# Optimization experiments

Measured on AMD Instinct MI355X. Metric: run time of the kernel, lower is better.

Reference implementation:

```python
import jax, jax.numpy as jnp
import numpy as np

EMBED_DIM = 256
NUM_HEADS = 8
HEAD_DIM = 32
INNER = NUM_HEADS * HEAD_DIM
NEG_SLOPE = 0.2


def setup_inputs() -> dict:
    key = jax.random.key(0)
    ks = jax.random.split(key, 8)
    B, Ns, Nt = 8, 1024, 1024
    src = jax.random.normal(ks[0], (B, Ns, EMBED_DIM), dtype=jnp.float32)
    trg = jax.random.normal(ks[1], (B, Nt, EMBED_DIM), dtype=jnp.float32)
    src_mask = jnp.ones((B, Ns), dtype=bool)
    trg_mask = jax.random.randint(ks[2], (B, Nt), 0, 2).astype(bool)
    # learned params (xavier-ish scale)
    def xavier(k, shape):
        fan_in, fan_out = shape[0], shape[-1]
        lim = (6.0 / (fan_in + fan_out)) ** 0.5
        return jax.random.uniform(k, shape, jnp.float32, -lim, lim)
    W_src = xavier(ks[3], (EMBED_DIM, INNER))
    W_trg = xavier(ks[4], (EMBED_DIM, INNER))  # is_cross_type=True -> independent
    a_src = xavier(ks[5], (NUM_HEADS, HEAD_DIM))
    a_trg = xavier(ks[6], (NUM_HEADS, HEAD_DIM))
    W_out = xavier(ks[7], (INNER, EMBED_DIM))
    return {"src": src, "trg": trg, "src_mask": src_mask, "trg_mask": trg_mask,
            "W_src": W_src, "W_trg": W_trg, "a_src": a_src, "a_trg": a_trg, "W_out": W_out}


def reference(src, trg, src_mask, trg_mask, W_src, W_trg, a_src, a_trg, W_out):
    B, Ns, _ = src.shape
    Nt = trg.shape[1]
    NH, Dh = NUM_HEADS, HEAD_DIM
    src_proj = (src @ W_src).reshape(B, Ns, NH, Dh)  # dropout p=0
    trg_proj = (trg @ W_trg).reshape(B, Nt, NH, Dh)
    score_src = jnp.einsum('bshd,hd->bsh', src_proj, a_src)
    score_trg = jnp.einsum('bthd,hd->bth', trg_proj, a_trg)
    # (B,Ns,NH,1) + (B,1,NH,Nt) -> (B,Ns,NH,Nt)
    scores = score_src[:, :, :, None] + jnp.transpose(score_trg, (0, 2, 1))[:, None, :, :]
    scores = jnp.where(scores >= 0, scores, NEG_SLOPE * scores)  # LeakyReLU
    edge_mask = src_mask[:, :, None, None] & trg_mask[:, None, None, :]
    scores = jnp.where(edge_mask, scores, -jnp.inf)
    attn = jax.nn.softmax(scores, axis=-1)
    attn = jnp.nan_to_num(attn, nan=0.0)
    aggregated = jnp.einsum('bsht,bthd->bshd', attn, trg_proj)
    output = aggregated.reshape(B, Ns, NH * Dh) @ W_out
    return output, jnp.transpose(attn, (0, 2, 1, 3))
```

## Files before the change

kernel.cpp:

```cpp
#include <hip/hip_runtime.h>
#include <hip/hip_bf16.h>
#include <math.h>

#define NB 8
#define NS 1024
#define NT 1024
#define NE 256
#define NHEADS 8
#define DH 32
#define LOG2E 1.4426950408889634f

typedef __attribute__((ext_vector_type(8))) short short8;
typedef __attribute__((ext_vector_type(8))) unsigned short ushort8;
typedef __attribute__((ext_vector_type(4))) float f32x4;

#define O_VT    0u
#define O_WTT   (8u<<20)
#define O_WTO   ((8u<<20)+131072u)
#define O_CSRC  ((8u<<20)+262144u)
#define O_CTRG  (O_CSRC+8192u)
#define O_SSRC  (O_CTRG+8192u)
#define O_STRG  (O_SSRC+262144u)
#define O_FLAG  (O_STRG+262144u)

__device__ __forceinline__ unsigned short f2bf(float f) {
    __hip_bfloat16 h = __float2bfloat16(f);
    union { __hip_bfloat16 h; unsigned short u; } c; c.h = h;
    return c.u;
}
__device__ __forceinline__ float leaky(float v) {
    return (v >= 0.f) ? v : 0.2f * v;
}
__device__ __forceinline__ float exp2_fast(float x) {
    float r;
    asm("v_exp_f32 %0, %1" : "=v"(r) : "v"(x));
    return r;
}

__global__ __launch_bounds__(256) void setup_kernel(
    const unsigned* __restrict__ tmask_dw, const float* __restrict__ Wsrc,
    const float* __restrict__ Wtrg, const float* __restrict__ Wout,
    const float* __restrict__ asrc, const float* __restrict__ atrg,
    float* __restrict__ c_src, float* __restrict__ c_trg,
    unsigned short* __restrict__ Wt_t, unsigned short* __restrict__ Wt_o,
    int* __restrict__ flag) {
    __shared__ __align__(16) char sm[16640];
    const int tid = threadIdx.x;
    const int bid = blockIdx.x;

    if (bid == 0) {
        __shared__ int s_ok;
        if (tid == 0) s_ok = 1;
        __syncthreads();
        for (int i = tid; i < 2048; i += 256)
            if (tmask_dw[i] > 1u) s_ok = 0;
        __syncthreads();
        if (tid == 0) *flag = s_ok;
    } else if (bid <= 2) {
        float* a_sh = (float*)sm;
        const float* W = (bid == 1) ? Wsrc : Wtrg;
        const float* a = (bid == 1) ? asrc : atrg;
        float* c = (bid == 1) ? c_src : c_trg;
        a_sh[tid] = a[tid];
        __syncthreads();
        const int e = tid;
        float ch[8];
#pragma unroll
        for (int h = 0; h < 8; ++h) ch[h] = 0.f;
        for (int i = 0; i < 64; ++i) {
            const float4 wv = *(const float4*)&W[(size_t)e * NE + i * 4];
            const int h = i >> 3, d0 = (i & 7) * 4;
            ch[h] += wv.x * a_sh[h * 32 + d0] + wv.y * a_sh[h * 32 + d0 + 1] +
                     wv.z * a_sh[h * 32 + d0 + 2] + wv.w * a_sh[h * 32 + d0 + 3];
        }
#pragma unroll
        for (int h = 0; h < 8; ++h) c[h * NE + e] = ch[h];
    } else {
        const int q = bid - 3;
        const float* W = (q >> 4) ? Wout : Wtrg;
        unsigned short* Wt = (q >> 4) ? Wt_o : Wt_t;
        const int tl = q & 15;
        const int k0 = (tl >> 2) * 64, n0 = (tl & 3) * 64;
        float* xs = (float*)sm;
#pragma unroll
        for (int it = 0; it < 4; ++it) {
            const int slot = it * 256 + tid;
            const int k = slot >> 4, c4 = slot & 15;
            const float4 v = *(const float4*)&W[(size_t)(k0 + k) * NE + n0 + c4 * 4];
            float* p = &xs[k * 65 + c4 * 4];
            p[0] = v.x; p[1] = v.y; p[2] = v.z; p[3] = v.w;
        }
        __syncthreads();
#pragma unroll
        for (int it = 0; it < 2; ++it) {
            const int slot = it * 256 + tid;
            const int n = slot >> 3, kc = slot & 7;
            ushort8 v;
#pragma unroll
            for (int e = 0; e < 8; ++e)
                v[e] = f2bf(xs[(kc * 8 + e) * 65 + n]);
            *(ushort8*)&Wt[(size_t)(n0 + n) * NE + k0 + kc * 8] = v;
        }
    }
}

__global__ __launch_bounds__(256) void mid_kernel(
    const float* __restrict__ src, const float* __restrict__ trg,
    const float* __restrict__ c_src, const float* __restrict__ c_trg,
    const unsigned short* __restrict__ Wt_t, unsigned short* __restrict__ Vt,
    float* __restrict__ ssrc, float* __restrict__ strg) {
    __shared__ __align__(16) char sm[49152];
    const int tid = threadIdx.x;
    const int bid = blockIdx.x;

    if (bid < 256) {
        unsigned short* As = (unsigned short*)sm;
        unsigned short* ldsT = (unsigned short*)(sm + 32768);
        const int lane = tid & 63, w = tid >> 6;
        const int row0 = (bid >> 1) * 64;
        const int col0 = (bid & 1) * 128;

#pragma unroll
        for (int it = 0; it < 8; ++it) {
            const int gf = it * 256 + tid;
            const int row = gf >> 5, g3 = gf & 31;
            const float4 a = *(const float4*)&trg[(size_t)(row0 + row) * NE + g3 * 8];
            const float4 b = *(const float4*)&trg[(size_t)(row0 + row) * NE + g3 * 8 + 4];
            ushort8 v;
            v[0] = f2bf(a.x); v[1] = f2bf(a.y); v[2] = f2bf(a.z); v[3] = f2bf(a.w);
            v[4] = f2bf(b.x); v[5] = f2bf(b.y); v[6] = f2bf(b.z); v[7] = f2bf(b.w);
            *(ushort8*)&As[row * NE + ((g3 ^ (row & 7)) * 8)] = v;
        }
        __syncthreads();

        const int r = lane & 15, g = lane >> 4;
        short8 af[8];
#pragma unroll
        for (int kk = 0; kk < 8; ++kk)
            af[kk] = *(const short8*)&As[(w * 16 + r) * NE + (((kk * 4 + g) ^ (r & 7)) * 8)];

        f32x4 acc[8];
#pragma unroll
        for (int nt = 0; nt < 8; ++nt) acc[nt] = (f32x4){0.f, 0.f, 0.f, 0.f};
#pragma unroll
        for (int kk = 0; kk < 8; ++kk) {
#pragma unroll
            for (int nt = 0; nt < 8; ++nt) {
                const int col = col0 + nt * 16 + r;
                const short8 bf = *(const short8*)&Wt_t[(size_t)col * NE + kk * 32 + g * 8];
                acc[nt] = __builtin_amdgcn_mfma_f32_16x16x32_bf16(af[kk], bf, acc[nt], 0, 0, 0);
            }
        }
        __syncthreads();

#pragma unroll
        for (int nt = 0; nt < 8; ++nt) {
            const int cl = nt * 16 + r;
            const int sw = (cl & 7) << 3;
#pragma unroll
            for (int j = 0; j < 4; ++j) {
                const int t = w * 16 + g * 4 + j;
                ldsT[cl * 64 + (t ^ sw)] = f2bf(acc[nt][j]);
            }
        }
        __syncthreads();

        const int b = row0 >> 10, t0 = row0 & 1023;
#pragma unroll
        for (int it = 0; it < 4; ++it) {
            const int slot = it * 256 + tid;
            const int cl = slot >> 3, ch = slot & 7;
            const int colg = col0 + cl;
            const int h = colg >> 5, d = colg & 31;
            *(ushort8*)&Vt[(((size_t)(b * 8 + h)) * 32 + d) * 1024 + t0 + ch * 8] =
                *(const ushort8*)&ldsT[cl * 64 + ch * 8];
        }
    } else {
        float* xs = (float*)sm;
        float* cs = (float*)(sm + 32768);
        const int rowg0 = (bid - 256) * 32;
        const bool is_src = rowg0 < NB * NS;
        const float* X = is_src ? (src + (size_t)rowg0 * NE)
                                : (trg + (size_t)(rowg0 - NB * NS) * NE);
        const float* C = is_src ? c_src : c_trg;
        float* S = is_src ? (ssrc + (size_t)rowg0 * NHEADS)
                          : (strg + (size_t)(rowg0 - NB * NS) * NHEADS);

#pragma unroll
        for (int it = 0; it < 8; ++it) {
            const int slot = it * 256 + tid;
            const int row = slot >> 6, c4 = slot & 63;
            *(float4*)&xs[row * NE + c4 * 4] =
                *(const float4*)&X[(size_t)row * NE + c4 * 4];
            cs[slot] = C[slot];
        }
        __syncthreads();

        const int r = tid >> 3, h = tid & 7;
        float s = 0.f;
        for (int e = 0; e < NE; e += 4) {
            const float4 x = *(const float4*)&xs[r * NE + e];
            const float4 c = *(const float4*)&cs[h * NE + e];
            s += x.x * c.x + x.y * c.y + x.z * c.z + x.w * c.w;
        }
        S[(size_t)r * NHEADS + h] = s;
    }
}

__global__ __launch_bounds__(256) void fused_kernel(
    const float* __restrict__ ssrc, const float* __restrict__ strg,
    const void* __restrict__ smask, const void* __restrict__ tmask,
    const int* __restrict__ flag_p, const unsigned short* __restrict__ Vt,
    const unsigned short* __restrict__ Wt_o,
    float* __restrict__ attn, float* __restrict__ out) {
    const int blk = blockIdx.x;
    const int q = blk & 63;
    const int b = blk >> 6;
    const int tid = threadIdx.x;
    const int lane = tid & 63;
    const int w = tid >> 6;
    const int flag = *flag_p;

    __shared__ __align__(16) float s_sm[8][1024];
    __shared__ __align__(16) unsigned short agg_sw[16 * 256];
    __shared__ float s_inv[8][16];
    __shared__ float s_ssv[8][16];

    for (int t = tid; t < NT; t += 256) {
        const bool mv = flag ? (((const int*)tmask)[b * NT + t] != 0)
                             : (((const unsigned char*)tmask)[b * NT + t] != 0);
        const float4 s0 = *(const float4*)&strg[((size_t)b * NT + t) * 8];
        const float4 s1 = *(const float4*)&strg[((size_t)b * NT + t) * 8 + 4];
        const float sv[8] = {s0.x, s0.y, s0.z, s0.w, s1.x, s1.y, s1.z, s1.w};
#pragma unroll
        for (int h = 0; h < 8; ++h)
            s_sm[h][t] = mv ? sv[h] * LOG2E : -1e30f;
    }
    __syncthreads();

    const int r = lane & 15;
    const int g = lane >> 4;
    const int srow = q * 16 + r;
    const bool rowv = flag ? (((const int*)smask)[b * NS + srow] != 0)
                           : (((const unsigned char*)smask)[b * NS + srow] != 0);
    const int sw = (r & 7) << 3;

    f32x4 acc0[2], acc1[2];

#pragma unroll
    for (int hh = 0; hh < 2; ++hh) {
        const int h = w * 2 + hh;
        const float ss2 = ssrc[((size_t)b * NS + srow) * NHEADS + h] * LOG2E;
        const unsigned short* vr0 = Vt + (size_t)(b * 8 + h) * 32768 + r * 1024;
        const unsigned short* vr1 = vr0 + 16 * 1024;
        f32x4 a0 = {0.f, 0.f, 0.f, 0.f};
        f32x4 a1 = {0.f, 0.f, 0.f, 0.f};
        float sum = 0.f;
#pragma unroll 4
        for (int c = 0; c < 32; ++c) {
            const int tb = c * 32 + g * 8;
            const short8 b0 = *(const short8*)&vr0[tb ^ sw];
            const short8 b1 = *(const short8*)&vr1[tb ^ sw];
            const float4 v0 = *(const float4*)&s_sm[h][tb];
            const float4 v1 = *(const float4*)&s_sm[h][tb + 4];
            const float vv[8] = {v0.x, v0.y, v0.z, v0.w, v1.x, v1.y, v1.z, v1.w};
            short8 pa;
#pragma unroll
            for (int e = 0; e < 8; ++e) {
                const float p = exp2_fast(leaky(ss2 + vv[e]));
                sum += p;
                pa[e] = (short)f2bf(p);
            }
            a0 = __builtin_amdgcn_mfma_f32_16x16x32_bf16(pa, b0, a0, 0, 0, 0);
            a1 = __builtin_amdgcn_mfma_f32_16x16x32_bf16(pa, b1, a1, 0, 0, 0);
        }
        sum += __shfl_xor(sum, 16);
        sum += __shfl_xor(sum, 32);
        const float inv = (rowv && sum > 0.f) ? 1.f / sum : 0.f;
        if (g == 0) {
            s_inv[h][r] = inv;
            s_ssv[h][r] = ss2;
        }
        acc0[hh] = a0;
        acc1[hh] = a1;
    }
    __syncthreads();

#pragma unroll
    for (int hh = 0; hh < 2; ++hh) {
        const int h = w * 2 + hh;
#pragma unroll
        for (int j = 0; j < 4; ++j) {
            const int row = g * 4 + j;
            const float iv = s_inv[h][row];
            int col = h * 32 + r;
            agg_sw[row * 256 + ((((col >> 3) ^ (row & 7)) << 3) | (col & 7))] =
                f2bf(acc0[hh][j] * iv);
            col += 16;
            agg_sw[row * 256 + ((((col >> 3) ^ (row & 7)) << 3) | (col & 7))] =
                f2bf(acc1[hh][j] * iv);
        }
    }
    __syncthreads();

    f32x4 oacc[4];
#pragma unroll
    for (int nt = 0; nt < 4; ++nt) oacc[nt] = (f32x4){0.f, 0.f, 0.f, 0.f};
#pragma unroll
    for (int kk = 0; kk < 8; ++kk) {
        const short8 af = *(const short8*)&agg_sw[r * 256 + (((kk * 4 + g) ^ (r & 7)) * 8)];
#pragma unroll
        for (int nt = 0; nt < 4; ++nt) {
            const int col = w * 64 + nt * 16 + r;
            const short8 bf = *(const short8*)&Wt_o[(size_t)col * NE + kk * 32 + g * 8];
            oacc[nt] = __builtin_amdgcn_mfma_f32_16x16x32_bf16(af, bf, oacc[nt], 0, 0, 0);
        }
    }
#pragma unroll
    for (int nt = 0; nt < 4; ++nt) {
        const int col = w * 64 + nt * 16 + r;
#pragma unroll
        for (int j = 0; j < 4; ++j)
            out[((size_t)b * NS + q * 16 + g * 4 + j) * NE + col] = oacc[nt][j];
    }

    for (int i = 0; i < 32; ++i) {
        const int idx = w * 32 + i;
        const int h = idx >> 4, rr = idx & 15;
        const float ssr = s_ssv[h][rr];
        const float ivr = s_inv[h][rr];
        float* arow = attn + ((size_t)(b * NHEADS + h) * NS + q * 16 + rr) * NT;
#pragma unroll
        for (int qq = 0; qq < 4; ++qq) {
            const int t0 = qq * 256 + lane * 4;
            const float4 sm4 = *(const float4*)&s_sm[h][t0];
            float4 o;
            o.x = exp2_fast(leaky(ssr + sm4.x)) * ivr;
            o.y = exp2_fast(leaky(ssr + sm4.y)) * ivr;
            o.z = exp2_fast(leaky(ssr + sm4.z)) * ivr;
            o.w = exp2_fast(leaky(ssr + sm4.w)) * ivr;
            *(float4*)&arow[t0] = o;
        }
    }
}

extern "C" void kernel_launch(void* const* d_in, const int* in_sizes, int n_in,
                              void* d_out, int out_size, void* d_ws, size_t ws_size,
                              hipStream_t stream) {
    const float* src   = (const float*)d_in[0];
    const float* trg   = (const float*)d_in[1];
    const void*  smask = d_in[2];
    const void*  tmask = d_in[3];
    const float* Wsrc  = (const float*)d_in[4];
    const float* Wtrg  = (const float*)d_in[5];
    const float* asrc  = (const float*)d_in[6];
    const float* atrg  = (const float*)d_in[7];
    const float* Wout  = (const float*)d_in[8];

    float* out  = (float*)d_out;
    float* attn = out + (size_t)NB * NS * NE;

    char* wsb = (char*)d_ws;
    unsigned short* Vt   = (unsigned short*)(wsb + O_VT);
    unsigned short* Wt_t = (unsigned short*)(wsb + O_WTT);
    unsigned short* Wt_o = (unsigned short*)(wsb + O_WTO);
    float* c_src = (float*)(wsb + O_CSRC);
    float* c_trg = (float*)(wsb + O_CTRG);
    float* ssrc  = (float*)(wsb + O_SSRC);
    float* strg  = (float*)(wsb + O_STRG);
    int*   flag  = (int*)(wsb + O_FLAG);

    setup_kernel<<<35, 256, 0, stream>>>(
        (const unsigned*)tmask, Wsrc, Wtrg, Wout, asrc, atrg,
        c_src, c_trg, Wt_t, Wt_o, flag);

    mid_kernel<<<768, 256, 0, stream>>>(
        src, trg, c_src, c_trg, Wt_t, Vt, ssrc, strg);

    fused_kernel<<<NB * (NS / 16), 256, 0, stream>>>(
        ssrc, strg, smask, tmask, flag, Vt, Wt_o, attn, out);
}
```

Measured before the change: 98.16 us.

## Replace dense attention aggregation with sorted prefix-sum decomposition of leaky softmax

The score is an additive rank-1 term passed through a LeakyReLU, so each branch factors into a product of a source term and a target term. Target scores are sorted per (batch, head). Exponential weights and their weighted V sums are prefix-scanned, and each source row binary-searches its split point to read the aggregated vector and the softmax normaliser in O(1). This removes the O(Ns*Nt) exp and MFMA work from aggregation. The attention matrix is now written as a select between precomputed per-target factors times per-row factors. The cost is a new low-parallelism sort/scan kernel with serial 1024-step scans, fp32 V staging, extra workspace traffic, and a possible risk of exponent overflow for extreme scores.

After: 207.6 us. +111.5%, slower.

```diff
diff --git a/kernel.cpp b/kernel.cpp
--- a/kernel.cpp
+++ b/kernel.cpp
@@ -14,22 +14,24 @@
 typedef __attribute__((ext_vector_type(8))) unsigned short ushort8;
 typedef __attribute__((ext_vector_type(4))) float f32x4;
 
-#define O_VT    0u
-#define O_WTT   (8u<<20)
-#define O_WTO   ((8u<<20)+131072u)
-#define O_CSRC  ((8u<<20)+262144u)
-#define O_CTRG  (O_CSRC+8192u)
-#define O_SSRC  (O_CTRG+8192u)
-#define O_STRG  (O_SSRC+262144u)
-#define O_FLAG  (O_STRG+262144u)
+#define O_V     0x0000000u
+#define O_T1    0x0800000u
+#define O_T2    0x1010000u
+#define O_EST1  0x1820000u
+#define O_EST2  0x1860000u
+#define O_RF    0x18A0000u
+#define O_WTT   0x19A0000u
+#define O_WTO   0x19C0000u
+#define O_CSRC  0x19E0000u
+#define O_CTRG  0x19E2000u
+#define O_SSRC  0x19E4000u
+#define O_STRG  0x1A24000u
+#define O_FLAG  0x1A64000u
 
 __device__ __forceinline__ unsigned short f2bf(float f) {
     __hip_bfloat16 h = __float2bfloat16(f);
     union { __hip_bfloat16 h; unsigned short u; } c; c.h = h;
     return c.u;
-}
-__device__ __forceinline__ float leaky(float v) {
-    return (v >= 0.f) ? v : 0.2f * v;
 }
 __device__ __forceinline__ float exp2_fast(float x) {
     float r;
@@ -107,15 +109,14 @@
 __global__ __launch_bounds__(256) void mid_kernel(
     const float* __restrict__ src, const float* __restrict__ trg,
     const float* __restrict__ c_src, const float* __restrict__ c_trg,
-    const unsigned short* __restrict__ Wt_t, unsigned short* __restrict__ Vt,
+    const unsigned short* __restrict__ Wt_t, float* __restrict__ Vg,
     float* __restrict__ ssrc, float* __restrict__ strg) {
-    __shared__ __align__(16) char sm[49152];
+    __shared__ __align__(16) char sm[40960];
     const int tid = threadIdx.x;
     const int bid = blockIdx.x;
 
     if (bid < 256) {
         unsigned short* As = (unsigned short*)sm;
-        unsigned short* ldsT = (unsigned short*)(sm + 32768);
         const int lane = tid & 63, w = tid >> 6;
         const int row0 = (bid >> 1) * 64;
         const int col0 = (bid & 1) * 128;
@@ -151,29 +152,17 @@
                 acc[nt] = __builtin_amdgcn_mfma_f32_16x16x32_bf16(af[kk], bf, acc[nt], 0, 0, 0);
             }
         }
-        __syncthreads();
-
+
+        const int b = row0 >> 10;
+        const int tloc = (row0 & 1023) + w * 16 + g * 4;
 #pragma unroll
         for (int nt = 0; nt < 8; ++nt) {
-            const int cl = nt * 16 + r;
-            const int sw = (cl & 7) << 3;
-#pragma unroll
-            for (int j = 0; j < 4; ++j) {
-                const int t = w * 16 + g * 4 + j;
-                ldsT[cl * 64 + (t ^ sw)] = f2bf(acc[nt][j]);
-            }
-        }
-        __syncthreads();
-
-        const int b = row0 >> 10, t0 = row0 & 1023;
-#pragma unroll
-        for (int it = 0; it < 4; ++it) {
-            const int slot = it * 256 + tid;
-            const int cl = slot >> 3, ch = slot & 7;
-            const int colg = col0 + cl;
-            const int h = colg >> 5, d = colg & 31;
-            *(ushort8*)&Vt[(((size_t)(b * 8 + h)) * 32 + d) * 1024 + t0 + ch * 8] =
-                *(const ushort8*)&ldsT[cl * 64 + ch * 8];
+            const int col = col0 + nt * 16 + r;
+            const int h = col >> 5, d = col & 31;
+            float* vb = Vg + ((size_t)(b * 8 + h) * 1024 + tloc) * 32 + d;
+#pragma unroll
+            for (int j = 0; j < 4; ++j)
+                vb[(size_t)j * 32] = acc[nt][j];
         }
     } else {
         float* xs = (float*)sm;
@@ -207,11 +196,147 @@
     }
 }
 
-__global__ __launch_bounds__(256) void fused_kernel(
+__global__ __launch_bounds__(256) void sortscan_kernel(
     const float* __restrict__ ssrc, const float* __restrict__ strg,
     const void* __restrict__ smask, const void* __restrict__ tmask,
-    const int* __restrict__ flag_p, const unsigned short* __restrict__ Vt,
-    const unsigned short* __restrict__ Wt_o,
+    const int* __restrict__ flag_p, const float* __restrict__ Vg,
+    float* __restrict__ T1g, float* __restrict__ T2g,
+    float* __restrict__ est1g, float* __restrict__ est2g,
+    float4* __restrict__ rfg) {
+    const int bid = blockIdx.x;
+    const int b = bid >> 3, h = bid & 7;
+    const int tid = threadIdx.x;
+    const int lane = tid & 63;
+    const int w = tid >> 6;
+    const int flag = *flag_p;
+    const float INF = __int_as_float(0x7f800000);
+
+    __shared__ float skey[1024];
+    __shared__ int   sidx[1024];
+    __shared__ float w1[1024], w2[1024];
+    __shared__ float sS1[1025], sS2[1025];
+    __shared__ float s_redm[4];
+    __shared__ int   s_redc[4];
+    __shared__ float s_Smax;
+
+    float lmax = -INF;
+    int lcnt = 0;
+    for (int t = tid; t < 1024; t += 256) {
+        const bool mv = flag ? (((const int*)tmask)[b * 1024 + t] != 0)
+                             : (((const unsigned char*)tmask)[b * 1024 + t] != 0);
+        const float S = strg[((size_t)b * 1024 + t) * 8 + h] * LOG2E;
+        skey[t] = mv ? S : INF;
+        sidx[t] = t;
+        if (mv) { lmax = fmaxf(lmax, S); ++lcnt; }
+    }
+#pragma unroll
+    for (int off = 32; off >= 1; off >>= 1) {
+        lmax = fmaxf(lmax, __shfl_xor(lmax, off));
+        lcnt += __shfl_xor(lcnt, off);
+    }
+    if (lane == 0) { s_redm[w] = lmax; s_redc[w] = lcnt; }
+    __syncthreads();
+    if (tid == 0) {
+        float m = fmaxf(fmaxf(s_redm[0], s_redm[1]), fmaxf(s_redm[2], s_redm[3]));
+        int c = s_redc[0] + s_redc[1] + s_redc[2] + s_redc[3];
+        s_Smax = (c > 0) ? m : 0.f;
+    }
+    __syncthreads();
+    const float Smax = s_Smax;
+
+    for (int kk = 2; kk <= 1024; kk <<= 1) {
+        for (int jj = kk >> 1; jj > 0; jj >>= 1) {
+            __syncthreads();
+            for (int ii = tid; ii < 1024; ii += 256) {
+                const int pr = ii ^ jj;
+                if (pr > ii) {
+                    const bool up = ((ii & kk) == 0);
+                    const float a = skey[ii], c = skey[pr];
+                    if (up ? (a > c) : (a < c)) {
+                        skey[ii] = c; skey[pr] = a;
+                        const int t = sidx[ii]; sidx[ii] = sidx[pr]; sidx[pr] = t;
+                    }
+                }
+            }
+        }
+    }
+    __syncthreads();
+
+    for (int j = tid; j < 1024; j += 256) {
+        const float sk = skey[j];
+        const bool valid = sk < 1e30f;
+        w1[j] = valid ? exp2_fast(sk - Smax) : 0.f;
+        w2[j] = valid ? exp2_fast(0.2f * (sk - Smax)) : 0.f;
+    }
+    __syncthreads();
+
+    if (w == 0) {
+        const int hf = lane >> 5, d = lane & 31;
+        float* Tb = (hf ? T2g : T1g) + (size_t)bid * 1025 * 32;
+        if (!hf) Tb[(size_t)1024 * 32 + d] = 0.f;
+        float acc = 0.f;
+        for (int j = 0; j < 1024; ++j) {
+            const int idx = hf ? j : 1023 - j;
+            const int perm = sidx[idx];
+            const float wv = hf ? w2[idx] : w1[idx];
+            const float vv = Vg[((size_t)bid * 1024 + perm) * 32 + d];
+            const float pre = acc;
+            acc = fmaf(wv, vv, acc);
+            Tb[(size_t)idx * 32 + d] = hf ? pre : acc;
+        }
+        if (hf) Tb[(size_t)1024 * 32 + d] = acc;
+    } else if (w == 1) {
+        const int hf = lane >> 5;
+        float acc = 0.f;
+        if (lane == 0) sS1[1024] = 0.f;
+        for (int j = 0; j < 1024; ++j) {
+            const int idx = hf ? j : 1023 - j;
+            const float wv = hf ? w2[idx] : w1[idx];
+            const float pre = acc;
+            acc += wv;
+            if ((lane & 31) == 0) (hf ? sS2 : sS1)[idx] = hf ? pre : acc;
+        }
+        if (lane == 32) sS2[1024] = acc;
+    } else {
+        for (int t = tid - 128; t < 1024; t += 128) {
+            const bool mv = flag ? (((const int*)tmask)[b * 1024 + t] != 0)
+                                 : (((const unsigned char*)tmask)[b * 1024 + t] != 0);
+            const float S = strg[((size_t)b * 1024 + t) * 8 + h] * LOG2E;
+            est1g[(size_t)bid * 1024 + t] = mv ? exp2_fast(S - Smax) : 0.f;
+            est2g[(size_t)bid * 1024 + t] = mv ? exp2_fast(0.2f * (S - Smax)) : 0.f;
+        }
+    }
+    __syncthreads();
+
+    for (int s = tid; s < 1024; s += 256) {
+        const float SS = ssrc[((size_t)b * 1024 + s) * 8 + h] * LOG2E;
+        const bool rowv = flag ? (((const int*)smask)[b * 1024 + s] != 0)
+                               : (((const unsigned char*)smask)[b * 1024 + s] != 0);
+        const float key = -SS;
+        int lo = 0, hi = 1024;
+        while (lo < hi) {
+            const int mid = (lo + hi) >> 1;
+            if (skey[mid] < key) lo = mid + 1; else hi = mid;
+        }
+        const int k = lo;
+        const float SSp = SS + Smax;
+        const float e1 = exp2_fast(SSp);
+        const float e2 = exp2_fast(0.2f * SSp);
+        const float sum = e1 * sS1[k] + e2 * sS2[k];
+        const float inv = (rowv && sum > 0.f) ? 1.f / sum : 0.f;
+        float4 rf;
+        rf.x = e1 * inv;
+        rf.y = e2 * inv;
+        rf.z = exp2_fast(-SSp);
+        rf.w = __int_as_float(k);
+        rfg[(size_t)bid * 1024 + s] = rf;
+    }
+}
+
+__global__ __launch_bounds__(256) void attnout_kernel(
+    const float4* __restrict__ rfg, const float* __restrict__ T1g,
+    const float* __restrict__ T2g, const float* __restrict__ est1g,
+    const float* __restrict__ est2g, const unsigned short* __restrict__ Wt_o,
     float* __restrict__ attn, float* __restrict__ out) {
     const int blk = blockIdx.x;
     const int q = blk & 63;
@@ -219,90 +344,32 @@
     const int tid = threadIdx.x;
     const int lane = tid & 63;
     const int w = tid >> 6;
-    const int flag = *flag_p;
-
-    __shared__ __align__(16) float s_sm[8][1024];
+
+    __shared__ float4 s_rf[8][16];
     __shared__ __align__(16) unsigned short agg_sw[16 * 256];
-    __shared__ float s_inv[8][16];
-    __shared__ float s_ssv[8][16];
-
-    for (int t = tid; t < NT; t += 256) {
-        const bool mv = flag ? (((const int*)tmask)[b * NT + t] != 0)
-                             : (((const unsigned char*)tmask)[b * NT + t] != 0);
-        const float4 s0 = *(const float4*)&strg[((size_t)b * NT + t) * 8];
-        const float4 s1 = *(const float4*)&strg[((size_t)b * NT + t) * 8 + 4];
-        const float sv[8] = {s0.x, s0.y, s0.z, s0.w, s1.x, s1.y, s1.z, s1.w};
-#pragma unroll
-        for (int h = 0; h < 8; ++h)
-            s_sm[h][t] = mv ? sv[h] * LOG2E : -1e30f;
-    }
-    __syncthreads();
-
-    const int r = lane & 15;
-    const int g = lane >> 4;
-    const int srow = q * 16 + r;
-    const bool rowv = flag ? (((const int*)smask)[b * NS + srow] != 0)
-                           : (((const unsigned char*)smask)[b * NS + srow] != 0);
-    const int sw = (r & 7) << 3;
-
-    f32x4 acc0[2], acc1[2];
-
-#pragma unroll
-    for (int hh = 0; hh < 2; ++hh) {
-        const int h = w * 2 + hh;
-        const float ss2 = ssrc[((size_t)b * NS + srow) * NHEADS + h] * LOG2E;
-        const unsigned short* vr0 = Vt + (size_t)(b * 8 + h) * 32768 + r * 1024;
-        const unsigned short* vr1 = vr0 + 16 * 1024;
-        f32x4 a0 = {0.f, 0.f, 0.f, 0.f};
-        f32x4 a1 = {0.f, 0.f, 0.f, 0.f};
-        float sum = 0.f;
-#pragma unroll 4
-        for (int c = 0; c < 32; ++c) {
-            const int tb = c * 32 + g * 8;
-            const short8 b0 = *(const short8*)&vr0[tb ^ sw];
-            const short8 b1 = *(const short8*)&vr1[tb ^ sw];
-            const float4 v0 = *(const float4*)&s_sm[h][tb];
-            const float4 v1 = *(const float4*)&s_sm[h][tb + 4];
-            const float vv[8] = {v0.x, v0.y, v0.z, v0.w, v1.x, v1.y, v1.z, v1.w};
-            short8 pa;
-#pragma unroll
-            for (int e = 0; e < 8; ++e) {
-                const float p = exp2_fast(leaky(ss2 + vv[e]));
-                sum += p;
-                pa[e] = (short)f2bf(p);
-            }
-            a0 = __builtin_amdgcn_mfma_f32_16x16x32_bf16(pa, b0, a0, 0, 0, 0);
-            a1 = __builtin_amdgcn_mfma_f32_16x16x32_bf16(pa, b1, a1, 0, 0, 0);
-        }
-        sum += __shfl_xor(sum, 16);
-        sum += __shfl_xor(sum, 32);
-        const float inv = (rowv && sum > 0.f) ? 1.f / sum : 0.f;
-        if (g == 0) {
-            s_inv[h][r] = inv;
-            s_ssv[h][r] = ss2;
-        }
-        acc0[hh] = a0;
-        acc1[hh] = a1;
-    }
-    __syncthreads();
-
-#pragma unroll
-    for (int hh = 0; hh < 2; ++hh) {
-        const int h = w * 2 + hh;
-#pragma unroll
-        for (int j = 0; j < 4; ++j) {
-            const int row = g * 4 + j;
-            const float iv = s_inv[h][row];
-            int col = h * 32 + r;
-            agg_sw[row * 256 + ((((col >> 3) ^ (row & 7)) << 3) | (col & 7))] =
-                f2bf(acc0[hh][j] * iv);
-            col += 16;
-            agg_sw[row * 256 + ((((col >> 3) ^ (row & 7)) << 3) | (col & 7))] =
-                f2bf(acc1[hh][j] * iv);
-        }
-    }
-    __syncthreads();
-
+
+    if (tid < 128) {
+        const int h = tid >> 4, r = tid & 15;
+        s_rf[h][r] = rfg[(size_t)(b * 8 + h) * 1024 + q * 16 + r];
+    }
+    __syncthreads();
+
+    {
+        const int h = tid >> 5, d = tid & 31;
+        const size_t tb = (size_t)(b * 8 + h) * 1025 * 32 + d;
+#pragma unroll
+        for (int r = 0; r < 16; ++r) {
+            const float4 rf = s_rf[h][r];
+            const int k = __float_as_int(rf.w);
+            const float a = rf.x * T1g[tb + (size_t)k * 32] +
+                            rf.y * T2g[tb + (size_t)k * 32];
+            const int col = h * 32 + d;
+            agg_sw[r * 256 + ((((col >> 3) ^ (r & 7)) << 3) | (col & 7))] = f2bf(a);
+        }
+    }
+    __syncthreads();
+
+    const int r = lane & 15, g = lane >> 4;
     f32x4 oacc[4];
 #pragma unroll
     for (int nt = 0; nt < 4; ++nt) oacc[nt] = (f32x4){0.f, 0.f, 0.f, 0.f};
@@ -327,18 +394,20 @@
     for (int i = 0; i < 32; ++i) {
         const int idx = w * 32 + i;
         const int h = idx >> 4, rr = idx & 15;
-        const float ssr = s_ssv[h][rr];
-        const float ivr = s_inv[h][rr];
+        const float4 rf = s_rf[h][rr];
+        const float* e1 = est1g + (size_t)(b * 8 + h) * 1024;
+        const float* e2 = est2g + (size_t)(b * 8 + h) * 1024;
         float* arow = attn + ((size_t)(b * NHEADS + h) * NS + q * 16 + rr) * NT;
 #pragma unroll
         for (int qq = 0; qq < 4; ++qq) {
             const int t0 = qq * 256 + lane * 4;
-            const float4 sm4 = *(const float4*)&s_sm[h][t0];
+            const float4 a1 = *(const float4*)&e1[t0];
+            const float4 a2 = *(const float4*)&e2[t0];
             float4 o;
-            o.x = exp2_fast(leaky(ssr + sm4.x)) * ivr;
-            o.y = exp2_fast(leaky(ssr + sm4.y)) * ivr;
-            o.z = exp2_fast(leaky(ssr + sm4.z)) * ivr;
-            o.w = exp2_fast(leaky(ssr + sm4.w)) * ivr;
+            o.x = (a1.x >= rf.z) ? a1.x * rf.x : a2.x * rf.y;
+            o.y = (a1.y >= rf.z) ? a1.y * rf.x : a2.y * rf.y;
+            o.z = (a1.z >= rf.z) ? a1.z * rf.x : a2.z * rf.y;
+            o.w = (a1.w >= rf.z) ? a1.w * rf.x : a2.w * rf.y;
             *(float4*)&arow[t0] = o;
         }
     }
@@ -361,7 +430,12 @@
     float* attn = out + (size_t)NB * NS * NE;
 
     char* wsb = (char*)d_ws;
-    unsigned short* Vt   = (unsigned short*)(wsb + O_VT);
+    float* Vg    = (float*)(wsb + O_V);
+    float* T1g   = (float*)(wsb + O_T1);
+    float* T2g   = (float*)(wsb + O_T2);
+    float* est1g = (float*)(wsb + O_EST1);
+    float* est2g = (float*)(wsb + O_EST2);
+    float4* rfg  = (float4*)(wsb + O_RF);
     unsigned short* Wt_t = (unsigned short*)(wsb + O_WTT);
     unsigned short* Wt_o = (unsigned short*)(wsb + O_WTO);
     float* c_src = (float*)(wsb + O_CSRC);
@@ -375,8 +449,11 @@
         c_src, c_trg, Wt_t, Wt_o, flag);
 
     mid_kernel<<<768, 256, 0, stream>>>(
-        src, trg, c_src, c_trg, Wt_t, Vt, ssrc, strg);
-
-    fused_kernel<<<NB * (NS / 16), 256, 0, stream>>>(
-        ssrc, strg, smask, tmask, flag, Vt, Wt_o, attn, out);
-}
+        src, trg, c_src, c_trg, Wt_t, Vg, ssrc, strg);
+
+    sortscan_kernel<<<NB * NHEADS, 256, 0, stream>>>(
+        ssrc, strg, smask, tmask, flag, Vg, T1g, T2g, est1g, est2g, rfg);
+
+    attnout_kernel<<<NB * (NS / 16), 256, 0, stream>>>(
+        rfg, T1g, T2g, est1g, est2g, Wt_o, attn, out);
+}
```

## Use 512-thread blocks with one wave per head in fused attention kernel

Applied to the files above, without the earlier changes.

Doubles the fused kernel's block size to 512 threads so each of the 8 waves handles a single head, rather than 4 waves each looping over two heads. The output projection tiles are split across 8 waves, and the attention write-back fetches per-row scores and inverse sums through wave shuffles instead of shared memory. This is meant to raise parallelism and latency hiding per block and to cut serial per-wave work. The cost is larger blocks, which may reduce the number of resident blocks per CU, plus a different register budget under the new launch bounds.

Measured after the change: 98.19 us. About the same (+0.0%).

```diff
diff --git a/kernel.cpp b/kernel.cpp
--- a/kernel.cpp
+++ b/kernel.cpp
@@ -207,7 +207,7 @@
     }
 }
 
-__global__ __launch_bounds__(256) void fused_kernel(
+__global__ __launch_bounds__(512) void fused_kernel(
     const float* __restrict__ ssrc, const float* __restrict__ strg,
     const void* __restrict__ smask, const void* __restrict__ tmask,
     const int* __restrict__ flag_p, const unsigned short* __restrict__ Vt,
@@ -224,9 +224,8 @@
     __shared__ __align__(16) float s_sm[8][1024];
     __shared__ __align__(16) unsigned short agg_sw[16 * 256];
     __shared__ float s_inv[8][16];
-    __shared__ float s_ssv[8][16];
-
-    for (int t = tid; t < NT; t += 256) {
+
+    for (int t = tid; t < NT; t += 512) {
         const bool mv = flag ? (((const int*)tmask)[b * NT + t] != 0)
                              : (((const unsigned char*)tmask)[b * NT + t] != 0);
         const float4 s0 = *(const float4*)&strg[((size_t)b * NT + t) * 8];
@@ -244,92 +243,77 @@
     const bool rowv = flag ? (((const int*)smask)[b * NS + srow] != 0)
                            : (((const unsigned char*)smask)[b * NS + srow] != 0);
     const int sw = (r & 7) << 3;
-
-    f32x4 acc0[2], acc1[2];
-
-#pragma unroll
-    for (int hh = 0; hh < 2; ++hh) {
-        const int h = w * 2 + hh;
-        const float ss2 = ssrc[((size_t)b * NS + srow) * NHEADS + h] * LOG2E;
-        const unsigned short* vr0 = Vt + (size_t)(b * 8 + h) * 32768 + r * 1024;
-        const unsigned short* vr1 = vr0 + 16 * 1024;
-        f32x4 a0 = {0.f, 0.f, 0.f, 0.f};
-        f32x4 a1 = {0.f, 0.f, 0.f, 0.f};
-        float sum = 0.f;
+    const int h = w;
+    const float ss2 = ssrc[((size_t)b * NS + srow) * NHEADS + h] * LOG2E;
+    const unsigned short* vr0 = Vt + (size_t)(b * 8 + h) * 32768 + r * 1024;
+    const unsigned short* vr1 = vr0 + 16 * 1024;
+
+    f32x4 acc0 = {0.f, 0.f, 0.f, 0.f};
+    f32x4 acc1 = {0.f, 0.f, 0.f, 0.f};
+    float sum = 0.f;
 #pragma unroll 4
-        for (int c = 0; c < 32; ++c) {
-            const int tb = c * 32 + g * 8;
-            const short8 b0 = *(const short8*)&vr0[tb ^ sw];
-            const short8 b1 = *(const short8*)&vr1[tb ^ sw];
-            const float4 v0 = *(const float4*)&s_sm[h][tb];
-            const float4 v1 = *(const float4*)&s_sm[h][tb + 4];
-            const float vv[8] = {v0.x, v0.y, v0.z, v0.w, v1.x, v1.y, v1.z, v1.w};
-            short8 pa;
-#pragma unroll
-            for (int e = 0; e < 8; ++e) {
-                const float p = exp2_fast(leaky(ss2 + vv[e]));
-                sum += p;
-                pa[e] = (short)f2bf(p);
-            }
-            a0 = __builtin_amdgcn_mfma_f32_16x16x32_bf16(pa, b0, a0, 0, 0, 0);
-            a1 = __builtin_amdgcn_mfma_f32_16x16x32_bf16(pa, b1, a1, 0, 0, 0);
-        }
-        sum += __shfl_xor(sum, 16);
-        sum += __shfl_xor(sum, 32);
-        const float inv = (rowv && sum > 0.f) ? 1.f / sum : 0.f;
-        if (g == 0) {
-            s_inv[h][r] = inv;
-            s_ssv[h][r] = ss2;
-        }
-        acc0[hh] = a0;
-        acc1[hh] = a1;
-    }
+    for (int c = 0; c < 32; ++c) {
+        const int tb = c * 32 + g * 8;
+        const short8 b0 = *(const short8*)&vr0[tb ^ sw];
+        const short8 b1 = *(const short8*)&vr1[tb ^ sw];
+        const float4 v0 = *(const float4*)&s_sm[h][tb];
+        const float4 v1 = *(const float4*)&s_sm[h][tb + 4];
+        const float vv[8] = {v0.x, v0.y, v0.z, v0.w, v1.x, v1.y, v1.z, v1.w};
+        short8 pa;
+#pragma unroll
+        for (int e = 0; e < 8; ++e) {
+            const float p = exp2_fast(leaky(ss2 + vv[e]));
+            sum += p;
+            pa[e] = (short)f2bf(p);
+        }
+        acc0 = __builtin_amdgcn_mfma_f32_16x16x32_bf16(pa, b0, acc0, 0, 0, 0);
+        acc1 = __builtin_amdgcn_mfma_f32_16x16x32_bf16(pa, b1, acc1, 0, 0, 0);
+    }
+    sum += __shfl_xor(sum, 16);
+    sum += __shfl_xor(sum, 32);
+    const float inv = (rowv && sum > 0.f) ? 1.f / sum : 0.f;
+    if (g == 0) s_inv[h][r] = inv;
     __syncthreads();
 
 #pragma unroll
-    for (int hh = 0; hh < 2; ++hh) {
-        const int h = w * 2 + hh;
-#pragma unroll
-        for (int j = 0; j < 4; ++j) {
-            const int row = g * 4 + j;
-            const float iv = s_inv[h][row];
-            int col = h * 32 + r;
-            agg_sw[row * 256 + ((((col >> 3) ^ (row & 7)) << 3) | (col & 7))] =
-                f2bf(acc0[hh][j] * iv);
-            col += 16;
-            agg_sw[row * 256 + ((((col >> 3) ^ (row & 7)) << 3) | (col & 7))] =
-                f2bf(acc1[hh][j] * iv);
-        }
+    for (int j = 0; j < 4; ++j) {
+        const int row = g * 4 + j;
+        const float iv = s_inv[h][row];
+        int col = h * 32 + r;
+        agg_sw[row * 256 + ((((col >> 3) ^ (row & 7)) << 3) | (col & 7))] =
+            f2bf(acc0[j] * iv);
+        col += 16;
+        agg_sw[row * 256 + ((((col >> 3) ^ (row & 7)) << 3) | (col & 7))] =
+            f2bf(acc1[j] * iv);
     }
     __syncthreads();
 
-    f32x4 oacc[4];
-#pragma unroll
-    for (int nt = 0; nt < 4; ++nt) oacc[nt] = (f32x4){0.f, 0.f, 0.f, 0.f};
+    f32x4 oacc[2];
+#pragma unroll
+    for (int nt = 0; nt < 2; ++nt) oacc[nt] = (f32x4){0.f, 0.f, 0.f, 0.f};
 #pragma unroll
     for (int kk = 0; kk < 8; ++kk) {
         const short8 af = *(const short8*)&agg_sw[r * 256 + (((kk * 4 + g) ^ (r & 7)) * 8)];
 #pragma unroll
-        for (int nt = 0; nt < 4; ++nt) {
-            const int col = w * 64 + nt * 16 + r;
+        for (int nt = 0; nt < 2; ++nt) {
+            const int col = w * 32 + nt * 16 + r;
             const short8 bf = *(const short8*)&Wt_o[(size_t)col * NE + kk * 32 + g * 8];
             oacc[nt] = __builtin_amdgcn_mfma_f32_16x16x32_bf16(af, bf, oacc[nt], 0, 0, 0);
         }
     }
 #pragma unroll
-    for (int nt = 0; nt < 4; ++nt) {
-        const int col = w * 64 + nt * 16 + r;
+    for (int nt = 0; nt < 2; ++nt) {
+        const int col = w * 32 + nt * 16 + r;
 #pragma unroll
         for (int j = 0; j < 4; ++j)
             out[((size_t)b * NS + q * 16 + g * 4 + j) * NE + col] = oacc[nt][j];
     }
 
-    for (int i = 0; i < 32; ++i) {
-        const int idx = w * 32 + i;
-        const int h = idx >> 4, rr = idx & 15;
-        const float ssr = s_ssv[h][rr];
-        const float ivr = s_inv[h][rr];
-        float* arow = attn + ((size_t)(b * NHEADS + h) * NS + q * 16 + rr) * NT;
+    float* wbase = attn + ((size_t)(b * NHEADS + h) * NS + q * 16) * NT;
+    for (int rr = 0; rr < 16; ++rr) {
+        const float ssr = __shfl(ss2, rr);
+        const float ivr = __shfl(inv, rr);
+        float* arow = wbase + (size_t)rr * NT;
 #pragma unroll
         for (int qq = 0; qq < 4; ++qq) {
             const int t0 = qq * 256 + lane * 4;
@@ -377,6 +361,6 @@
     mid_kernel<<<768, 256, 0, stream>>>(
         src, trg, c_src, c_trg, Wt_t, Vt, ssrc, strg);
 
-    fused_kernel<<<NB * (NS / 16), 256, 0, stream>>>(
+    fused_kernel<<<NB * (NS / 16), 512, 0, stream>>>(
         ssrc, strg, smask, tmask, flag, Vt, Wt_o, attn, out);
 }
```
